# Optimization experiments

Measured on AMD Instinct MI355X. Metric: run time of the kernel, lower is better.

Reference implementation:

```python
import jax, jax.numpy as jnp
import numpy as np

DIM = 1024
HEADS = 16
B, N = 4, 2048


def setup_inputs() -> dict:
    key = jax.random.key(0)
    ks = jax.random.split(key, 6)
    scale = DIM ** -0.5
    return {
        "x": jax.random.normal(ks[0], (B, N, DIM), dtype=jnp.float32),
        "mask": jax.random.randint(ks[1], (B, N, N), 0, 2) > 0,
        "Wqkv": jax.random.normal(ks[2], (DIM, 3 * DIM), dtype=jnp.float32) * scale,
        "bqkv": jax.random.normal(ks[3], (3 * DIM,), dtype=jnp.float32) * 0.02,
        "Wproj": jax.random.normal(ks[4], (DIM, DIM), dtype=jnp.float32) * scale,
        "bproj": jax.random.normal(ks[5], (DIM,), dtype=jnp.float32) * 0.02,
    }


def reference(x, mask, Wqkv, bqkv, Wproj, bproj):
    Bs, Ns, C = x.shape
    H = HEADS
    D = C // H
    scale = D ** -0.5
    qkv = x @ Wqkv + bqkv                       # [B, N, 3C]
    qkv = qkv.reshape(Bs, Ns, 3, H, D)          # split (three h d)
    q, k, v = jnp.moveaxis(qkv, 2, 0)           # each [B, N, H, D]
    q = q.transpose(0, 2, 1, 3)                 # [B, H, N, D]
    k = k.transpose(0, 2, 1, 3)
    v = v.transpose(0, 2, 1, 3)
    attn = jnp.einsum("bhnd,bhmd->bhnm", q, k) * scale  # [B, H, N, N]
    attn = jnp.where(mask[:, None, :, :], -jnp.inf, attn)
    attn = jax.nn.softmax(attn, axis=-1)
    out = jnp.einsum("bhnm,bhmd->bhnd", attn, v)        # [B, H, N, D]
    out = out.transpose(0, 2, 1, 3).reshape(Bs, Ns, C)  # [B, N, C]
    return out @ Wproj + bproj
```

## Files before the change

kernel.cpp:

```cpp
#include <hip/hip_runtime.h>
#include <cstdint>
#include <cstddef>

constexpr int kC = 1024;
constexpr int kH = 16;
constexpr int kB = 4;
constexpr int kN = 2048;
constexpr int kD = 64;

#define KQ_SCALE 0.18033688011112042f

typedef unsigned short u16;
typedef unsigned int   u32;
typedef unsigned long long u64;
typedef __bf16 v8bf  __attribute__((ext_vector_type(8)));
typedef __bf16 v4bf  __attribute__((ext_vector_type(4)));
typedef float  v4f   __attribute__((ext_vector_type(4)));
typedef u16    u16x8 __attribute__((ext_vector_type(8)));
typedef u16    u16x4 __attribute__((ext_vector_type(4)));
typedef u32    u32x4 __attribute__((ext_vector_type(4)));

__device__ inline u16 f2bf(float f) {
    union { float f; unsigned u; } v; v.f = f;
    unsigned r = v.u + 0x7FFFu + ((v.u >> 16) & 1u);
    return (u16)(r >> 16);
}

__device__ inline float fast_exp2(float x) {
#if __has_builtin(__builtin_amdgcn_exp2f)
    return __builtin_amdgcn_exp2f(x);
#else
    return __expf(x * 0.6931471805599453f);
#endif
}

__device__ inline void gl2lds16(const u16* g, u16* l) {
    __builtin_amdgcn_global_load_lds(
        (const __attribute__((address_space(1))) void*)g,
        (__attribute__((address_space(3))) void*)l, 16, 0, 0);
}

__global__ __launch_bounds__(256) void cast_bf16_kernel(
    const float* __restrict__ in, u16* __restrict__ outp)
{
    const int i = blockIdx.x * 256 + threadIdx.x;
    const float4 f = ((const float4*)in)[i];
    u16x4 o;
    o.x = f2bf(f.x); o.y = f2bf(f.y); o.z = f2bf(f.z); o.w = f2bf(f.w);
    ((u16x4*)outp)[i] = o;
}

__global__ __launch_bounds__(256) void tpose_cast_kernel(
    const float* __restrict__ W, u16* __restrict__ Wt, int R, int Cc)
{
    __shared__ u16 tile[64][65];
    const int c0 = blockIdx.x * 64;
    const int r0 = blockIdx.y * 64;
    const int t  = threadIdx.x;
#pragma unroll
    for (int it = 0; it < 16; ++it) {
        const int r = it * 4 + (t >> 6);
        const int c = t & 63;
        tile[c][r] = f2bf(W[(size_t)(r0 + r) * Cc + c0 + c]);
    }
    __syncthreads();
#pragma unroll
    for (int it = 0; it < 16; ++it) {
        const int rr = it * 4 + (t >> 6);
        const int cc = t & 63;
        Wt[(size_t)(c0 + rr) * R + r0 + cc] = tile[rr][cc];
    }
}

__global__ __launch_bounds__(256) void maskpack_kernel(
    const int* __restrict__ mask, u32* __restrict__ bits)
{
    const int seg  = blockIdx.x * 4 + (threadIdx.x >> 6);
    const int lane = threadIdx.x & 63;
    const size_t row = (size_t)(seg >> 5);
    const int s = seg & 31;
    const int m = mask[row * kN + s * 64 + lane];
    const u64 bal = __ballot(m != 0);
    if (lane == 0) ((u64*)bits)[row * 32 + s] = bal;
}

template <int MODE>
__global__ __launch_bounds__(256, 3) void gemm_mfma_kernel(
    const u16* __restrict__ A, const u16* __restrict__ Bt,
    const float* __restrict__ bias, float* __restrict__ Cout,
    u16* __restrict__ qOut, u16* __restrict__ kOut, u16* __restrict__ vOut,
    int M, int N, int K)
{
    __shared__ u16 As0[128 * 32], Bs0[128 * 32];
    __shared__ u16 As1[128 * 32], Bs1[128 * 32];
    __shared__ u16 As2[128 * 32], Bs2[128 * 32];
    const int t    = threadIdx.x;
    const int w    = t >> 6;
    const int lane = t & 63;
    const int quad = lane >> 4;
    const int l16  = lane & 15;

    const int nby = M >> 7;
    const int q8  = (int)gridDim.x >> 3;
    const int bid = (int)blockIdx.x;
    const int swz = (bid & 7) * q8 + (bid >> 3);
    const int m0  = (swz % nby) * 128;
    const int n0  = (swz / nby) * 128;

    const int sr  = lane >> 2;
    const int scs = ((lane & 3) ^ ((sr >> 1) & 3)) * 8;
    const u16* Ag0 = A  + (size_t)(m0 + 32 * w      + sr) * K + scs;
    const u16* Ag1 = A  + (size_t)(m0 + 32 * w + 16 + sr) * K + scs;
    const u16* Bg0 = Bt + (size_t)(n0 + 32 * w      + sr) * K + scs;
    const u16* Bg1 = Bt + (size_t)(n0 + 32 * w + 16 + sr) * K + scs;

    v4f acc[4][4];
#pragma unroll
    for (int r = 0; r < 4; ++r)
#pragma unroll
        for (int c = 0; c < 4; ++c) acc[r][c] = (v4f){0.f, 0.f, 0.f, 0.f};

    const int mrow = (w >> 1) * 64;
    const int ncol = (w & 1) * 64;
    const int pch  = (quad ^ ((l16 >> 1) & 3)) * 8;

    auto stage = [&](u16* Asb, u16* Bsb, int k0) {
        gl2lds16(Ag0 + k0, Asb + (32 * w) * 32);
        gl2lds16(Ag1 + k0, Asb + (32 * w + 16) * 32);
        gl2lds16(Bg0 + k0, Bsb + (32 * w) * 32);
        gl2lds16(Bg1 + k0, Bsb + (32 * w + 16) * 32);
    };
    auto compute = [&](const u16* Asb, const u16* Bsb) {
        v8bf af[4], bfr[4];
#pragma unroll
        for (int r = 0; r < 4; ++r)
            af[r] = *(const v8bf*)(Asb + (mrow + r * 16 + l16) * 32 + pch);
#pragma unroll
        for (int c = 0; c < 4; ++c)
            bfr[c] = *(const v8bf*)(Bsb + (ncol + c * 16 + l16) * 32 + pch);
        __builtin_amdgcn_s_setprio(1);
#pragma unroll
        for (int r = 0; r < 4; ++r)
#pragma unroll
            for (int c = 0; c < 4; ++c)
                acc[r][c] = __builtin_amdgcn_mfma_f32_16x16x32_bf16(
                    af[r], bfr[c], acc[r][c], 0, 0, 0);
        __builtin_amdgcn_s_setprio(0);
    };

    stage(As0, Bs0, 0);
    stage(As1, Bs1, 32);
    u16 *pa0 = As0, *pb0 = Bs0, *pa1 = As1, *pb1 = Bs1, *pa2 = As2, *pb2 = Bs2;

    for (int k0 = 0; k0 < K; k0 += 32) {
        if (k0 + 32 < K) {
            asm volatile("s_waitcnt vmcnt(4)" ::: "memory");
        } else {
            asm volatile("s_waitcnt vmcnt(0)" ::: "memory");
        }
        __builtin_amdgcn_s_barrier();
        __builtin_amdgcn_sched_barrier(0);
        if (k0 + 64 < K) stage(pa2, pb2, k0 + 64);
        compute(pa0, pb0);
        u16* ta = pa0; pa0 = pa1; pa1 = pa2; pa2 = ta;
        u16* tb = pb0; pb0 = pb1; pb1 = pb2; pb2 = tb;
    }

#pragma unroll
    for (int r = 0; r < 4; ++r) {
#pragma unroll
        for (int c = 0; c < 4; ++c) {
            const int col = n0 + ncol + c * 16 + l16;
            const float bv = bias[col];
#pragma unroll
            for (int reg = 0; reg < 4; ++reg) {
                const int row = m0 + mrow + r * 16 + quad * 4 + reg;
                float val = acc[r][c][reg] + bv;
                if (MODE == 0) {
                    Cout[(size_t)row * N + col] = val;
                } else {
                    const int which = col >> 10;
                    const int rem   = col & 1023;
                    const int h     = rem >> 6;
                    const int d     = rem & 63;
                    const int b     = row >> 11;
                    const int n     = row & 2047;
                    if (which == 0) val *= KQ_SCALE;
                    u16* dst = (which == 0) ? qOut : (which == 1) ? kOut : vOut;
                    dst[(((size_t)(b * kH + h)) * kN + n) * kD + d] = f2bf(val);
                }
            }
        }
    }
}

__global__ __launch_bounds__(256, 2) void attn_mfma_kernel(
    const u16* __restrict__ q, const u16* __restrict__ k,
    const u16* __restrict__ v, const u32* __restrict__ mbits,
    u16* __restrict__ out)
{
    __shared__ u16 Ks[128 * 64];
    __shared__ u16 Vt[64 * 128];

    const int t    = threadIdx.x;
    const int w    = t >> 6;
    const int lane = t & 63;
    const int quad = lane >> 4;
    const int l16  = lane & 15;

    const int bh    = blockIdx.x >> 4;
    const int tile0 = (blockIdx.x & 15) * 128;
    const int b     = bh >> 4;
    const int h     = bh & 15;

    const u16* qb = q + (size_t)bh * kN * kD;
    const u16* kb = k + (size_t)bh * kN * kD;
    const u16* vb = v + (size_t)bh * kN * kD;

    const int qrow0 = tile0 + w * 32 + l16;
    const int qrow1 = qrow0 + 16;
    v8bf qf[2][2];
    qf[0][0] = *(const v8bf*)(qb + (size_t)qrow0 * kD + quad * 8);
    qf[0][1] = *(const v8bf*)(qb + (size_t)qrow0 * kD + 32 + quad * 8);
    qf[1][0] = *(const v8bf*)(qb + (size_t)qrow1 * kD + quad * 8);
    qf[1][1] = *(const v8bf*)(qb + (size_t)qrow1 * kD + 32 + quad * 8);

    const int skr  = t >> 1;
    const int skh  = t & 1;
    const int vg   = t >> 4;
    const int vdq  = t & 15;
    const int vrow0 = (vg >> 2) * 32 + (vg & 3) * 4;

    const u16* kp = kb + (size_t)skr * kD + skh * 32;
    const u16* vp = vb + (size_t)vrow0 * kD + vdq * 4;
    const uint4* mp0 = (const uint4*)(mbits + ((size_t)b * kN + qrow0) * 64);
    const uint4* mp1 = (const uint4*)(mbits + ((size_t)b * kN + qrow1) * 64);

    u16x8 kpre[4];
    u16x4 vpre[8];
    uint4 mpre0, mpre1;
    auto issue_prefetch = [&]() {
#pragma unroll
        for (int i = 0; i < 4; ++i)
            kpre[i] = *(const u16x8*)(kp + i * 8);
#pragma unroll
        for (int i = 0; i < 8; ++i)
            vpre[i] = *(const u16x4*)(vp + (i < 4 ? i * 64 : 1024 + (i - 4) * 64));
        mpre0 = *mp0; mpre1 = *mp1;
        kp += 128 * kD; vp += 128 * kD; ++mp0; ++mp1;
    };

    v8bf onesf;
#pragma unroll
    for (int j = 0; j < 8; ++j) onesf[j] = (__bf16)1.0f;

    v4f oacc[2][4];
    v4f rsacc[2];
#pragma unroll
    for (int qs = 0; qs < 2; ++qs) {
        rsacc[qs] = (v4f){0.f, 0.f, 0.f, 0.f};
#pragma unroll
        for (int i = 0; i < 4; ++i) oacc[qs][i] = (v4f){0.f, 0.f, 0.f, 0.f};
    }

    issue_prefetch();

    for (int kt = 0; kt < kN / 128; ++kt) {
        __syncthreads();

        {
            const int cb = skh * 4;
            u16* drow = &Ks[skr * 64];
#pragma unroll
            for (int i = 0; i < 4; ++i)
                *(u16x8*)(&drow[((cb + i) ^ (skr & 7)) * 8]) = kpre[i];
        }
        {
#pragma unroll
            for (int dd = 0; dd < 4; ++dd) {
                const int d = vdq * 4 + dd;
                u16x8 col;
#pragma unroll
                for (int j = 0; j < 8; ++j) col[j] = vpre[j][dd];
                *(u16x8*)(&Vt[d * 128 + ((vg ^ (d & 15)) * 8)]) = col;
            }
        }
        const uint4 mc0 = mpre0, mc1 = mpre1;
        if (kt + 1 < kN / 128) issue_prefetch();
        __syncthreads();

        const u32 mwa[2][4] = {{mc0.x, mc0.y, mc0.z, mc0.w},
                               {mc1.x, mc1.y, mc1.z, mc1.w}};
        u32 pf[2][4][4];

#pragma unroll
        for (int nb = 0; nb < 8; ++nb) {
            const int krow = nb * 16 + l16;
            const v8bf kf0 = *(const v8bf*)(&Ks[krow * 64 + ((quad       ^ (krow & 7)) * 8)]);
            const v8bf kf1 = *(const v8bf*)(&Ks[krow * 64 + (((quad + 4) ^ (krow & 7)) * 8)]);
#pragma unroll
            for (int qs = 0; qs < 2; ++qs) {
                v4f s = (v4f){0.f, 0.f, 0.f, 0.f};
                s = __builtin_amdgcn_mfma_f32_16x16x32_bf16(kf0, qf[qs][0], s, 0, 0, 0);
                s = __builtin_amdgcn_mfma_f32_16x16x32_bf16(kf1, qf[qs][1], s, 0, 0, 0);

                const u32 m4 = (mwa[qs][nb >> 1] >> ((nb & 1) * 16 + quad * 4)) & 0xFu;
                float e0 = fast_exp2(s[0]);
                float e1 = fast_exp2(s[1]);
                float e2 = fast_exp2(s[2]);
                float e3 = fast_exp2(s[3]);
                e0 = (m4 & 1u) ? 0.f : e0;
                e1 = (m4 & 2u) ? 0.f : e1;
                e2 = (m4 & 4u) ? 0.f : e2;
                e3 = (m4 & 8u) ? 0.f : e3;

                union { v4bf v; u32 u[2]; } bu;
                bu.v = (v4bf){(__bf16)e0, (__bf16)e1, (__bf16)e2, (__bf16)e3};
                pf[qs][nb >> 1][(nb & 1) * 2 + 0] = bu.u[0];
                pf[qs][nb >> 1][(nb & 1) * 2 + 1] = bu.u[1];
            }
        }

        v8bf pa[2][4];
#pragma unroll
        for (int qs = 0; qs < 2; ++qs)
#pragma unroll
            for (int ks = 0; ks < 4; ++ks) {
                u32x4 t4 = {pf[qs][ks][0], pf[qs][ks][1], pf[qs][ks][2], pf[qs][ks][3]};
                pa[qs][ks] = __builtin_bit_cast(v8bf, t4);
            }

        __builtin_amdgcn_s_setprio(1);
#pragma unroll
        for (int qs = 0; qs < 2; ++qs)
#pragma unroll
            for (int ks = 0; ks < 4; ++ks)
                rsacc[qs] = __builtin_amdgcn_mfma_f32_16x16x32_bf16(
                    pa[qs][ks], onesf, rsacc[qs], 0, 0, 0);
#pragma unroll
        for (int ks = 0; ks < 4; ++ks)
#pragma unroll
            for (int db = 0; db < 4; ++db) {
                const int d = db * 16 + l16;
                const v8bf vf = *(const v8bf*)(&Vt[d * 128 + (((ks * 4 + quad) ^ (d & 15)) * 8)]);
#pragma unroll
                for (int qs = 0; qs < 2; ++qs)
                    oacc[qs][db] = __builtin_amdgcn_mfma_f32_16x16x32_bf16(
                        pa[qs][ks], vf, oacc[qs][db], 0, 0, 0);
            }
        __builtin_amdgcn_s_setprio(0);
    }

#pragma unroll
    for (int qs = 0; qs < 2; ++qs) {
        float inv[4];
#pragma unroll
        for (int reg = 0; reg < 4; ++reg) inv[reg] = 1.f / rsacc[qs][reg];
#pragma unroll
        for (int db = 0; db < 4; ++db)
#pragma unroll
            for (int reg = 0; reg < 4; ++reg) {
                const int row = tile0 + w * 32 + qs * 16 + quad * 4 + reg;
                const int col = h * 64 + db * 16 + l16;
                out[((size_t)(b * kN + row)) * kC + col] = f2bf(oacc[qs][db][reg] * inv[reg]);
            }
    }
}

extern "C" void kernel_launch(void* const* d_in, const int* in_sizes, int n_in,
                              void* d_out, int out_size, void* d_ws, size_t ws_size,
                              hipStream_t stream)
{
    const float* x     = (const float*)d_in[0];
    const int*   mask  = (const int*)d_in[1];
    const float* Wqkv  = (const float*)d_in[2];
    const float* bqkv  = (const float*)d_in[3];
    const float* Wproj = (const float*)d_in[4];
    const float* bproj = (const float*)d_in[5];
    float* out = (float*)d_out;

    const size_t nx = (size_t)kB * kN * kC;
    const size_t qkv_elems = (size_t)kB * kH * kN * kD;
    u16* xb     = (u16*)d_ws;
    u16* qbuf   = xb + nx;
    u16* kbuf   = qbuf + qkv_elems;
    u16* vbuf   = kbuf + qkv_elems;
    u16* aob    = vbuf + qkv_elems;
    u16* Wqkvt  = aob + nx;
    u16* Wprojt = Wqkvt + (size_t)3 * kC * kC;
    u32* mbits  = (u32*)(Wprojt + (size_t)kC * kC);

    maskpack_kernel<<<dim3(kB * kN * 32 / 4), dim3(256), 0, stream>>>(mask, mbits);
    cast_bf16_kernel<<<dim3(nx / 1024), dim3(256), 0, stream>>>(x, xb);
    tpose_cast_kernel<<<dim3(3 * kC / 64, kC / 64), dim3(256), 0, stream>>>(
        Wqkv, Wqkvt, kC, 3 * kC);
    tpose_cast_kernel<<<dim3(kC / 64, kC / 64), dim3(256), 0, stream>>>(
        Wproj, Wprojt, kC, kC);

    gemm_mfma_kernel<1><<<dim3((3 * kC / 128) * (kB * kN / 128)), dim3(256), 0, stream>>>(
        xb, Wqkvt, bqkv, nullptr, qbuf, kbuf, vbuf, kB * kN, 3 * kC, kC);

    attn_mfma_kernel<<<dim3(kB * kH * (kN / 128)), dim3(256), 0, stream>>>(
        qbuf, kbuf, vbuf, mbits, aob);

    gemm_mfma_kernel<0><<<dim3((kC / 128) * (kB * kN / 128)), dim3(256), 0, stream>>>(
        aob, Wprojt, bproj, out, nullptr, nullptr, nullptr, kB * kN, kC, kC);
}
```

Baseline: 375.4 us.

## Double-buffer K/V shared tiles in attention and grid-stride the mask pack

The attention kernel now keeps two LDS buffers for K and transposed V and alternates between them each key tile, which removes the barrier at the top of the loop. Only one __syncthreads per iteration remains. P fragments are written straight into the bf16 vectors, with no packing through u32 arrays. The mask packing kernel becomes a grid-stride loop over a fixed 2048-block grid. Doubling LDS to 64KB may reduce occupancy below the 2-blocks-per-SM hint, and one barrier per tile with two buffers is borderline safe for ordering.

```diff
diff --git a/kernel.cpp b/kernel.cpp
--- a/kernel.cpp
+++ b/kernel.cpp
@@ -75,13 +75,16 @@
 __global__ __launch_bounds__(256) void maskpack_kernel(
     const int* __restrict__ mask, u32* __restrict__ bits)
 {
-    const int seg  = blockIdx.x * 4 + (threadIdx.x >> 6);
     const int lane = threadIdx.x & 63;
-    const size_t row = (size_t)(seg >> 5);
-    const int s = seg & 31;
-    const int m = mask[row * kN + s * 64 + lane];
-    const u64 bal = __ballot(m != 0);
-    if (lane == 0) ((u64*)bits)[row * 32 + s] = bal;
+    const int wv   = threadIdx.x >> 6;
+    const int nseg = kB * kN * 32;
+    for (int seg = blockIdx.x * 4 + wv; seg < nseg; seg += gridDim.x * 4) {
+        const size_t row = (size_t)(seg >> 5);
+        const int s = seg & 31;
+        const int m = mask[row * kN + s * 64 + lane];
+        const u64 bal = __ballot(m != 0);
+        if (lane == 0) ((u64*)bits)[row * 32 + s] = bal;
+    }
 }
 
 template <int MODE>
@@ -199,8 +202,8 @@
     const u16* __restrict__ v, const u32* __restrict__ mbits,
     u16* __restrict__ out)
 {
-    __shared__ u16 Ks[128 * 64];
-    __shared__ u16 Vt[64 * 128];
+    __shared__ u16 Ks[2][128 * 64];
+    __shared__ u16 Vt[2][64 * 128];
 
     const int t    = threadIdx.x;
     const int w    = t >> 6;
@@ -266,11 +269,12 @@
     issue_prefetch();
 
     for (int kt = 0; kt < kN / 128; ++kt) {
-        __syncthreads();
+        u16* KsB = Ks[kt & 1];
+        u16* VtB = Vt[kt & 1];
 
         {
             const int cb = skh * 4;
-            u16* drow = &Ks[skr * 64];
+            u16* drow = &KsB[skr * 64];
 #pragma unroll
             for (int i = 0; i < 4; ++i)
                 *(u16x8*)(&drow[((cb + i) ^ (skr & 7)) * 8]) = kpre[i];
@@ -282,22 +286,23 @@
                 u16x8 col;
 #pragma unroll
                 for (int j = 0; j < 8; ++j) col[j] = vpre[j][dd];
-                *(u16x8*)(&Vt[d * 128 + ((vg ^ (d & 15)) * 8)]) = col;
+                *(u16x8*)(&VtB[d * 128 + ((vg ^ (d & 15)) * 8)]) = col;
             }
         }
         const uint4 mc0 = mpre0, mc1 = mpre1;
         if (kt + 1 < kN / 128) issue_prefetch();
+
         __syncthreads();
 
         const u32 mwa[2][4] = {{mc0.x, mc0.y, mc0.z, mc0.w},
                                {mc1.x, mc1.y, mc1.z, mc1.w}};
-        u32 pf[2][4][4];
+        v8bf pa[2][4];
 
 #pragma unroll
         for (int nb = 0; nb < 8; ++nb) {
             const int krow = nb * 16 + l16;
-            const v8bf kf0 = *(const v8bf*)(&Ks[krow * 64 + ((quad       ^ (krow & 7)) * 8)]);
-            const v8bf kf1 = *(const v8bf*)(&Ks[krow * 64 + (((quad + 4) ^ (krow & 7)) * 8)]);
+            const v8bf kf0 = *(const v8bf*)(&KsB[krow * 64 + ((quad       ^ (krow & 7)) * 8)]);
+            const v8bf kf1 = *(const v8bf*)(&KsB[krow * 64 + (((quad + 4) ^ (krow & 7)) * 8)]);
 #pragma unroll
             for (int qs = 0; qs < 2; ++qs) {
                 v4f s = (v4f){0.f, 0.f, 0.f, 0.f};
@@ -314,21 +319,12 @@
                 e2 = (m4 & 4u) ? 0.f : e2;
                 e3 = (m4 & 8u) ? 0.f : e3;
 
-                union { v4bf v; u32 u[2]; } bu;
-                bu.v = (v4bf){(__bf16)e0, (__bf16)e1, (__bf16)e2, (__bf16)e3};
-                pf[qs][nb >> 1][(nb & 1) * 2 + 0] = bu.u[0];
-                pf[qs][nb >> 1][(nb & 1) * 2 + 1] = bu.u[1];
+                pa[qs][nb >> 1][(nb & 1) * 4 + 0] = (__bf16)e0;
+                pa[qs][nb >> 1][(nb & 1) * 4 + 1] = (__bf16)e1;
+                pa[qs][nb >> 1][(nb & 1) * 4 + 2] = (__bf16)e2;
+                pa[qs][nb >> 1][(nb & 1) * 4 + 3] = (__bf16)e3;
             }
         }
-
-        v8bf pa[2][4];
-#pragma unroll
-        for (int qs = 0; qs < 2; ++qs)
-#pragma unroll
-            for (int ks = 0; ks < 4; ++ks) {
-                u32x4 t4 = {pf[qs][ks][0], pf[qs][ks][1], pf[qs][ks][2], pf[qs][ks][3]};
-                pa[qs][ks] = __builtin_bit_cast(v8bf, t4);
-            }
 
         __builtin_amdgcn_s_setprio(1);
 #pragma unroll
@@ -342,7 +338,7 @@
 #pragma unroll
             for (int db = 0; db < 4; ++db) {
                 const int d = db * 16 + l16;
-                const v8bf vf = *(const v8bf*)(&Vt[d * 128 + (((ks * 4 + quad) ^ (d & 15)) * 8)]);
+                const v8bf vf = *(const v8bf*)(&VtB[d * 128 + (((ks * 4 + quad) ^ (d & 15)) * 8)]);
 #pragma unroll
                 for (int qs = 0; qs < 2; ++qs)
                     oacc[qs][db] = __builtin_amdgcn_mfma_f32_16x16x32_bf16(
@@ -390,7 +386,7 @@
     u16* Wprojt = Wqkvt + (size_t)3 * kC * kC;
     u32* mbits  = (u32*)(Wprojt + (size_t)kC * kC);
 
-    maskpack_kernel<<<dim3(kB * kN * 32 / 4), dim3(256), 0, stream>>>(mask, mbits);
+    maskpack_kernel<<<dim3(2048), dim3(256), 0, stream>>>(mask, mbits);
     cast_bf16_kernel<<<dim3(nx / 1024), dim3(256), 0, stream>>>(x, xb);
     tpose_cast_kernel<<<dim3(3 * kC / 64, kC / 64), dim3(256), 0, stream>>>(
         Wqkv, Wqkvt, kC, 3 * kC);
```

Result: faster. 361.1 us (-3.8%).
